# Performance work log

Measured on AMD Instinct MI355X. Metric: run time of the kernel, lower is better.

Reference implementation:

```python
import jax, jax.numpy as jnp
import numpy as np
import math

EMBED_DIM = 1024
NUM_HEADS = 16
HEAD_DIM = EMBED_DIM // NUM_HEADS
SCALING = HEAD_DIM ** -0.5
SOFTPLUS_BETA = math.log(2.0)


def linear(x, W, b):
    # torch nn.Linear: x @ W.T + b
    return jnp.einsum('...i,oi->...o', x, W) + b


def efficient_causal_attention_parallel(x, y, z):
    # x: (B, n, d1), y: (B, n, d1), z: (B, n, d2)
    n = x.shape[1]
    # outer products per step, then causal prefix-sum over n
    accum = jnp.cumsum(jnp.einsum('bni,bnj->bnij', y, z), axis=1)  # (B, n, d1, d2)
    res = jnp.einsum('bni,bnij->bnj', x, accum)                    # (B, n, d2)
    length_div = jnp.arange(1, n + 1, dtype=x.dtype)[None, :, None]
    return res / length_div


def setup_inputs() -> dict:
    key = jax.random.key(0)
    ks = jax.random.split(key, 12)
    tgt_len, bsz, plen = 2048, 2, 32
    E = EMBED_DIM
    s = 1.0 / math.sqrt(E)
    return {
        'query': jax.random.normal(ks[0], (tgt_len, bsz, E), jnp.float32),
        'pquery': jax.random.normal(ks[1], (plen, bsz, E), jnp.float32),
        'Wpq': jax.random.normal(ks[2], (E, E), jnp.float32) * s,
        'bpq': jnp.zeros((E,), jnp.float32),
        'Wq': jax.random.normal(ks[3], (E, E), jnp.float32) * s,
        'bq': jnp.zeros((E,), jnp.float32),
        'Wpc': jax.random.normal(ks[4], (E, E), jnp.float32) * s,
        'bpc': jnp.zeros((E,), jnp.float32),
        'Wc': jax.random.normal(ks[5], (E, E), jnp.float32) * s,
        'bc': jnp.zeros((E,), jnp.float32),
        'Wo': jax.random.normal(ks[6], (E, E), jnp.float32) * s,
        'bo': jnp.zeros((E,), jnp.float32),
    }


def reference(query, pquery, Wpq, bpq, Wq, bq, Wpc, bpc, Wc, bc, Wo, bo):
    tgt_len, bsz, E = query.shape
    plen = pquery.shape[0]
    H, D = NUM_HEADS, HEAD_DIM
    BH = bsz * H

    # pq: (plen, bsz, E) -> (bsz, H, plen, D), scaled
    pq = linear(pquery, Wpq, bpq).reshape(plen, bsz, H, D)
    pq = jnp.transpose(pq, (1, 2, 0, 3)) * SCALING

    # _compute_pattention: k (BH, tgt_len, D) @ pq^T (BH, D, plen)
    kp = linear(query, Wpc, bpc).reshape(tgt_len, BH, D).transpose(1, 0, 2)
    pqm = pq.reshape(BH, plen, D).transpose(0, 2, 1)  # (BH, D, plen)
    pattn = jnp.matmul(kp, pqm)                        # (BH, tgt_len, plen)
    pattn = jax.nn.softplus(SOFTPLUS_BETA * pattn) / SOFTPLUS_BETA

    q = (linear(query, Wq, bq) * SCALING).reshape(tgt_len, BH, D).transpose(1, 0, 2)
    kv = linear(query, Wc, bc).reshape(tgt_len, BH, D).transpose(1, 0, 2)  # tied k=v

    attn_weights = efficient_causal_attention_parallel(q, kv, pattn)  # (BH, tgt_len, plen)
    attn_weights = jax.nn.softmax(attn_weights, axis=-1)
    attn = efficient_causal_attention_parallel(attn_weights, pattn, kv)  # (BH, tgt_len, D)

    attn = attn.transpose(1, 0, 2).reshape(tgt_len, bsz, E)
    return linear(attn, Wo, bo)
```

## Files before the change

### kernel.cpp

```cpp
#include <hip/hip_runtime.h>
#include <hip/hip_bf16.h>
#include <math.h>

typedef __hip_bfloat16 bf16;
typedef __attribute__((ext_vector_type(8))) short bf16x8;
typedef __attribute__((ext_vector_type(4))) float f32x4;

__device__ __forceinline__ float bfbits(unsigned int u){ union{unsigned int x; float f;} c; c.x = u; return c.f; }
__device__ __forceinline__ short f2bf_s(float v){ union{ bf16 b; short s;} u; u.b = __float2bfloat16(v); return u.s; }

__device__ __forceinline__ void gl_lds16(const bf16* g, short* l) {
    __builtin_amdgcn_global_load_lds(
        (const __attribute__((address_space(1))) void*)g,
        (__attribute__((address_space(3))) void*)l, 16, 0, 0);
}

#define LN2F 0.69314718055994531f

__device__ __forceinline__ void cvt_store4(bf16* d, size_t idx, float4 v) {
    union { ushort4 u; bf16 b[4]; } o;
    o.b[0] = __float2bfloat16(v.x);
    o.b[1] = __float2bfloat16(v.y);
    o.b[2] = __float2bfloat16(v.z);
    o.b[3] = __float2bfloat16(v.w);
    ((ushort4*)d)[idx] = o.u;
}

__global__ __launch_bounds__(256)
void conv1_kernel(const float* __restrict__ query, const float* __restrict__ pquery,
                  const float* __restrict__ Wpq, bf16* __restrict__ qbf,
                  bf16* __restrict__ pqy, bf16* __restrict__ wpq)
{
    int blk = blockIdx.x;
    const float* s; bf16* d; int i;
    if (blk < 4096)      { s = query;  d = qbf; i = blk * 256 + threadIdx.x; }
    else if (blk < 4160) { s = pquery; d = pqy; i = (blk - 4096) * 256 + threadIdx.x; }
    else                 { s = Wpq;    d = wpq; i = (blk - 4160) * 256 + threadIdx.x; }
    cvt_store4(d, i, ((const float4*)s)[i]);
}

__global__ __launch_bounds__(256)
void conv2_kernel(const float* __restrict__ Wpc, const float* __restrict__ Wq,
                  const float* __restrict__ Wc, const float* __restrict__ Wo,
                  const float* __restrict__ bpc, const float* __restrict__ bq,
                  const float* __restrict__ bc,
                  bf16* __restrict__ wcat, bf16* __restrict__ wo_bf,
                  float* __restrict__ biascat)
{
    int blk = blockIdx.x;
    if (blk < 3072) {
        const float* s = (blk < 1024) ? Wpc : ((blk < 2048) ? Wq : Wc);
        int rel = (blk & 1023) * 256 + threadIdx.x;
        bf16* d = wcat + (size_t)(blk >> 10) * 1048576;
        cvt_store4(d, rel, ((const float4*)s)[rel]);
    } else if (blk < 4096) {
        int rel = (blk - 3072) * 256 + threadIdx.x;
        cvt_store4(wo_bf, rel, ((const float4*)Wo)[rel]);
    } else {
        int i = (blk - 4096) * 256 + threadIdx.x;
        float v = (i < 1024) ? bpc[i] : ((i < 2048) ? bq[i - 1024] : bc[i - 2048]);
        biascat[i] = v;
    }
}

__global__ __launch_bounds__(256)
void gemm_bf16_nt(const bf16* __restrict__ A, const bf16* __restrict__ B,
                  const float* __restrict__ bias, float* __restrict__ C,
                  int M, int N, int K, float scale_all, float scale_mid)
{
    __shared__ short As[128 * 32];
    __shared__ short Bs[128 * 32];

    const int tid  = threadIdx.x;
    const int lane = tid & 63;
    const int wave = tid >> 6;
    const int m0 = blockIdx.y * 128;
    const int n0 = blockIdx.x * 128;
    const int wm = (wave >> 1) * 64;
    const int wn = (wave & 1) * 64;

    f32x4 acc[4][4] = {};

    const int c0 = tid, c1 = tid + 256;
    const int r0 = c0 >> 2, s0 = c0 & 3;
    const int r1 = c1 >> 2, s1 = c1 & 3;

    const int kb = lane >> 4;
    const int rr = lane & 15;

    for (int k0 = 0; k0 < K; k0 += 32) {
        __syncthreads();
        gl_lds16(A + (size_t)(m0 + r0) * K + k0 + s0 * 8, As + c0 * 8);
        gl_lds16(A + (size_t)(m0 + r1) * K + k0 + s1 * 8, As + c1 * 8);
        gl_lds16(B + (size_t)(n0 + r0) * K + k0 + s0 * 8, Bs + c0 * 8);
        gl_lds16(B + (size_t)(n0 + r1) * K + k0 + s1 * 8, Bs + c1 * 8);
        __syncthreads();

        bf16x8 af[4], bfr[4];
        #pragma unroll
        for (int mi = 0; mi < 4; ++mi)
            af[mi] = *(const bf16x8*)(As + (wm + mi * 16 + rr) * 32 + kb * 8);
        #pragma unroll
        for (int ni = 0; ni < 4; ++ni)
            bfr[ni] = *(const bf16x8*)(Bs + (wn + ni * 16 + rr) * 32 + kb * 8);
        #pragma unroll
        for (int mi = 0; mi < 4; ++mi)
            #pragma unroll
            for (int ni = 0; ni < 4; ++ni)
                acc[mi][ni] = __builtin_amdgcn_mfma_f32_16x16x32_bf16(
                    af[mi], bfr[ni], acc[mi][ni], 0, 0, 0);
    }

    const int col_l = lane & 15;
    const int row_q = lane >> 4;
    #pragma unroll
    for (int ni = 0; ni < 4; ++ni) {
        int col = n0 + wn + ni * 16 + col_l;
        float bb = bias[col];
        float sc = ((col >> 10) == 1) ? scale_mid : scale_all;
        #pragma unroll
        for (int mi = 0; mi < 4; ++mi) {
            #pragma unroll
            for (int r = 0; r < 4; ++r) {
                int row = m0 + wm + mi * 16 + row_q * 4 + r;
                C[(size_t)row * N + col] = sc * (acc[mi][ni][r] + bb);
            }
        }
    }
}

__global__ __launch_bounds__(256)
void gemm_pq_partial(const bf16* __restrict__ A, const bf16* __restrict__ B,
                     float* __restrict__ part)
{
    __shared__ short As[64 * 32];
    __shared__ short Bs[128 * 32];

    const int tid  = threadIdx.x;
    const int lane = tid & 63;
    const int wave = tid >> 6;
    const int n0 = blockIdx.x * 128;
    const int kslice = blockIdx.y;
    const int kbase = kslice * 128;

    f32x4 acc[4][2] = {};

    const int ra = tid >> 2, sa = tid & 3;
    const int c0 = tid, c1 = tid + 256;
    const int rb0 = c0 >> 2, sb0 = c0 & 3;
    const int rb1 = c1 >> 2, sb1 = c1 & 3;

    const int kb = lane >> 4;
    const int rr = lane & 15;

    for (int k0 = kbase; k0 < kbase + 128; k0 += 32) {
        __syncthreads();
        gl_lds16(A + (size_t)ra * 1024 + k0 + sa * 8, As + tid * 8);
        gl_lds16(B + (size_t)(n0 + rb0) * 1024 + k0 + sb0 * 8, Bs + c0 * 8);
        gl_lds16(B + (size_t)(n0 + rb1) * 1024 + k0 + sb1 * 8, Bs + c1 * 8);
        __syncthreads();

        bf16x8 af[4], bfr[2];
        #pragma unroll
        for (int mi = 0; mi < 4; ++mi)
            af[mi] = *(const bf16x8*)(As + (mi * 16 + rr) * 32 + kb * 8);
        #pragma unroll
        for (int ni = 0; ni < 2; ++ni)
            bfr[ni] = *(const bf16x8*)(Bs + (wave * 32 + ni * 16 + rr) * 32 + kb * 8);
        #pragma unroll
        for (int mi = 0; mi < 4; ++mi)
            #pragma unroll
            for (int ni = 0; ni < 2; ++ni)
                acc[mi][ni] = __builtin_amdgcn_mfma_f32_16x16x32_bf16(
                    af[mi], bfr[ni], acc[mi][ni], 0, 0, 0);
    }

    const int col_l = lane & 15;
    const int row_q = lane >> 4;
    float* dst = part + (size_t)kslice * 65536;
    #pragma unroll
    for (int ni = 0; ni < 2; ++ni) {
        int col = n0 + wave * 32 + ni * 16 + col_l;
        #pragma unroll
        for (int mi = 0; mi < 4; ++mi) {
            #pragma unroll
            for (int r = 0; r < 4; ++r) {
                int row = mi * 16 + row_q * 4 + r;
                dst[(size_t)row * 1024 + col] = acc[mi][ni][r];
            }
        }
    }
}

__global__ __launch_bounds__(256)
void pq_reduce(const float* __restrict__ part, const float* __restrict__ bias,
               float* __restrict__ pq)
{
    int gid = blockIdx.x * 256 + threadIdx.x;
    int n = gid & 1023;
    float s = bias[n];
    #pragma unroll
    for (int k = 0; k < 8; ++k) s += part[(size_t)k * 65536 + gid];
    pq[gid] = 0.125f * s;
}

__global__ __launch_bounds__(256)
void pattn_sum_kernel(const float* __restrict__ kp, const float* __restrict__ kv,
                      const float* __restrict__ pq, float* __restrict__ pattn,
                      float* __restrict__ Sbuf, int T, int ld)
{
    const int NCH = 32;
    const int c = blockIdx.x, bh = blockIdx.y;
    const int b = bh >> 4, h = bh & 15;
    const int t0 = c * 64;
    const int tid = threadIdx.x;
    __shared__ float pqs[32][65];
    __shared__ float kps[64][65];
    __shared__ float ps[64][33];
    float* kvs = &kps[0][0];

    #pragma unroll
    for (int l = 0; l < 8; ++l) {
        int idx = tid + l * 256;
        int p = idx >> 6, d = idx & 63;
        pqs[p][d] = pq[(size_t)(p * 2 + b) * 1024 + h * 64 + d];
    }
    #pragma unroll
    for (int l = 0; l < 16; ++l) {
        int idx = tid + l * 256;
        int t = idx >> 6, d = idx & 63;
        kps[t][d] = kp[(size_t)((t0 + t) * 2 + b) * ld + h * 64 + d];
    }
    __syncthreads();

    const int p = tid & 31, tb = tid >> 5;
    float spv[8];
    #pragma unroll
    for (int l = 0; l < 8; ++l) {
        int t = tb + l * 8;
        float dot = 0.f;
        for (int d = 0; d < 64; ++d) dot += kps[t][d] * pqs[p][d];
        float z = LN2F * dot;
        spv[l] = (fmaxf(z, 0.f) + log1pf(expf(-fabsf(z)))) / LN2F;
    }
    __syncthreads();

    #pragma unroll
    for (int l = 0; l < 8; ++l) {
        int t = tb + l * 8;
        ps[t][p] = spv[l];
        pattn[((size_t)bh * T + t0 + t) * 32 + p] = spv[l];
    }
    #pragma unroll
    for (int l = 0; l < 16; ++l) {
        int idx = tid + l * 256;
        int t = idx >> 6, d = idx & 63;
        kvs[t * 64 + d] = kv[(size_t)((t0 + t) * 2 + b) * ld + h * 64 + d];
    }
    __syncthreads();

    const int j = tid & 31;
    const int ib = tid >> 5;
    float acc[8] = {};
    for (int r = 0; r < 64; ++r) {
        float pj = ps[r][j];
        #pragma unroll
        for (int k = 0; k < 8; ++k) acc[k] += kvs[r * 64 + ib + 8 * k] * pj;
    }
    float* Sdst = Sbuf + ((size_t)bh * NCH + c) * 2048;
    #pragma unroll
    for (int k = 0; k < 8; ++k) Sdst[tid + k * 256] = acc[k];
}

__global__ __launch_bounds__(256)
void prefix_state_kernel(float* __restrict__ Sbuf)
{
    const int NCH = 32;
    int gid = blockIdx.x * 256 + threadIdx.x;
    int bh = gid >> 11, e = gid & 2047;
    float* p = Sbuf + (size_t)bh * NCH * 2048 + e;
    float run = 0.f;
    #pragma unroll
    for (int c = 0; c < NCH; ++c) {
        float t = p[c * 2048];
        p[c * 2048] = run;
        run += t;
    }
}

__global__ __launch_bounds__(256)
void chunk_attn(const float* __restrict__ qg, const float* __restrict__ kvg,
                const float* __restrict__ pg, const float* __restrict__ Sg,
                bf16* __restrict__ attn, int T, int ld)
{
    __shared__ short sm[30720];
    short* sQ   = sm;
    short* sKV  = sm + 4608;
    short* sKVT = sm + 9216;
    short* sW   = sm + 13824;
    short* sAW  = sm + 18432;
    short* sS   = sm + 20992;
    short* sST  = sm + 23552;
    short* sP   = sm + 25856;
    short* sPT  = sm + 28416;

    const int bh = blockIdx.y, c = blockIdx.x;
    const int b = bh >> 4, h = bh & 15;
    const int t0 = c * 64;
    const int tid = threadIdx.x;
    const int lane = tid & 63;
    const int wave = tid >> 6;
    const int rr = lane & 15;
    const int kb = lane >> 4;
    const int m0w = wave * 16;
    const float* Sblk = Sg + ((size_t)bh * 32 + c) * 2048;

    #pragma unroll
    for (int l = 0; l < 4; ++l) {
        int idx = tid + l * 256;
        int t = idx >> 4, d4 = (idx & 15) * 4;
        size_t g = (size_t)((t0 + t) * 2 + b) * ld + h * 64 + d4;
        float4 qv = *(const float4*)(qg + g);
        union { ushort4 u; short s[4]; bf16 bb[4]; } cq;
        cq.bb[0] = __float2bfloat16(qv.x);
        cq.bb[1] = __float2bfloat16(qv.y);
        cq.bb[2] = __float2bfloat16(qv.z);
        cq.bb[3] = __float2bfloat16(qv.w);
        *(ushort4*)(sQ + t * 72 + d4) = cq.u;
        float4 kvv = *(const float4*)(kvg + g);
        union { ushort4 u; short s[4]; bf16 bb[4]; } ck;
        ck.bb[0] = __float2bfloat16(kvv.x);
        ck.bb[1] = __float2bfloat16(kvv.y);
        ck.bb[2] = __float2bfloat16(kvv.z);
        ck.bb[3] = __float2bfloat16(kvv.w);
        *(ushort4*)(sKV + t * 72 + d4) = ck.u;
        #pragma unroll
        for (int i = 0; i < 4; ++i) sKVT[(d4 + i) * 72 + t] = ck.s[i];
    }
    #pragma unroll
    for (int l = 0; l < 2; ++l) {
        int idx = tid + l * 256;
        int i = idx >> 3, j4 = (idx & 7) * 4;
        float4 sv = *(const float4*)(Sblk + i * 32 + j4);
        union { ushort4 u; short s[4]; bf16 bb[4]; } cs;
        cs.bb[0] = __float2bfloat16(sv.x);
        cs.bb[1] = __float2bfloat16(sv.y);
        cs.bb[2] = __float2bfloat16(sv.z);
        cs.bb[3] = __float2bfloat16(sv.w);
        *(ushort4*)(sS + i * 40 + j4) = cs.u;
        #pragma unroll
        for (int k = 0; k < 4; ++k) sST[(j4 + k) * 72 + i] = cs.s[k];
        float4 pv = *(const float4*)(pg + ((size_t)bh * T + t0 + i) * 32 + j4);
        union { ushort4 u; short s[4]; bf16 bb[4]; } cp;
        cp.bb[0] = __float2bfloat16(pv.x);
        cp.bb[1] = __float2bfloat16(pv.y);
        cp.bb[2] = __float2bfloat16(pv.z);
        cp.bb[3] = __float2bfloat16(pv.w);
        *(ushort4*)(sP + i * 40 + j4) = cp.u;
        #pragma unroll
        for (int k = 0; k < 4; ++k) sPT[(j4 + k) * 72 + i] = cp.s[k];
    }
    __syncthreads();

    {
        bf16x8 aq0 = *(const bf16x8*)(sQ + (m0w + rr) * 72 + kb * 8);
        bf16x8 aq1 = *(const bf16x8*)(sQ + (m0w + rr) * 72 + 32 + kb * 8);
        f32x4 acc[4] = {};
        #pragma unroll
        for (int nt = 0; nt < 4; ++nt) {
            bf16x8 b0 = *(const bf16x8*)(sKV + (nt * 16 + rr) * 72 + kb * 8);
            bf16x8 b1 = *(const bf16x8*)(sKV + (nt * 16 + rr) * 72 + 32 + kb * 8);
            acc[nt] = __builtin_amdgcn_mfma_f32_16x16x32_bf16(aq0, b0, acc[nt], 0, 0, 0);
            acc[nt] = __builtin_amdgcn_mfma_f32_16x16x32_bf16(aq1, b1, acc[nt], 0, 0, 0);
        }
        #pragma unroll
        for (int nt = 0; nt < 4; ++nt)
            #pragma unroll
            for (int r = 0; r < 4; ++r) {
                int t = m0w + kb * 4 + r;
                int s = nt * 16 + rr;
                sW[t * 72 + s] = f2bf_s((s <= t) ? acc[nt][r] : 0.f);
            }
    }
    __syncthreads();

    {
        bf16x8 aq0 = *(const bf16x8*)(sQ + (m0w + rr) * 72 + kb * 8);
        bf16x8 aq1 = *(const bf16x8*)(sQ + (m0w + rr) * 72 + 32 + kb * 8);
        bf16x8 aw0 = *(const bf16x8*)(sW + (m0w + rr) * 72 + kb * 8);
        bf16x8 aw1 = *(const bf16x8*)(sW + (m0w + rr) * 72 + 32 + kb * 8);
        f32x4 acc[2] = {};
        #pragma unroll
        for (int nt = 0; nt < 2; ++nt) {
            bf16x8 bs0 = *(const bf16x8*)(sST + (nt * 16 + rr) * 72 + kb * 8);
            bf16x8 bs1 = *(const bf16x8*)(sST + (nt * 16 + rr) * 72 + 32 + kb * 8);
            bf16x8 bp0 = *(const bf16x8*)(sPT + (nt * 16 + rr) * 72 + kb * 8);
            bf16x8 bp1 = *(const bf16x8*)(sPT + (nt * 16 + rr) * 72 + 32 + kb * 8);
            acc[nt] = __builtin_amdgcn_mfma_f32_16x16x32_bf16(aq0, bs0, acc[nt], 0, 0, 0);
            acc[nt] = __builtin_amdgcn_mfma_f32_16x16x32_bf16(aq1, bs1, acc[nt], 0, 0, 0);
            acc[nt] = __builtin_amdgcn_mfma_f32_16x16x32_bf16(aw0, bp0, acc[nt], 0, 0, 0);
            acc[nt] = __builtin_amdgcn_mfma_f32_16x16x32_bf16(aw1, bp1, acc[nt], 0, 0, 0);
        }
        #pragma unroll
        for (int r = 0; r < 4; ++r) {
            int t = m0w + kb * 4 + r;
            float inv_len = 1.0f / (float)(t0 + t + 1);
            float v0 = acc[0][r] * inv_len;
            float v1 = acc[1][r] * inv_len;
            float m = fmaxf(v0, v1);
            m = fmaxf(m, __shfl_xor(m, 1));
            m = fmaxf(m, __shfl_xor(m, 2));
            m = fmaxf(m, __shfl_xor(m, 4));
            m = fmaxf(m, __shfl_xor(m, 8));
            float e0 = __expf(v0 - m), e1 = __expf(v1 - m);
            float s = e0 + e1;
            s += __shfl_xor(s, 1);
            s += __shfl_xor(s, 2);
            s += __shfl_xor(s, 4);
            s += __shfl_xor(s, 8);
            float rs = 1.0f / s;
            sAW[t * 40 + rr]      = f2bf_s(e0 * rs);
            sAW[t * 40 + 16 + rr] = f2bf_s(e1 * rs);
        }
    }
    __syncthreads();

    {
        bf16x8 aa = *(const bf16x8*)(sAW + (m0w + rr) * 40 + kb * 8);
        f32x4 acc[4] = {};
        #pragma unroll
        for (int nt = 0; nt < 4; ++nt) {
            bf16x8 bp = *(const bf16x8*)(sP + (nt * 16 + rr) * 40 + kb * 8);
            acc[nt] = __builtin_amdgcn_mfma_f32_16x16x32_bf16(aa, bp, acc[nt], 0, 0, 0);
        }
        __syncthreads();
        #pragma unroll
        for (int nt = 0; nt < 4; ++nt)
            #pragma unroll
            for (int r = 0; r < 4; ++r) {
                int t = m0w + kb * 4 + r;
                int s = nt * 16 + rr;
                sW[t * 72 + s] = f2bf_s((s <= t) ? acc[nt][r] : 0.f);
            }
    }
    __syncthreads();

    {
        bf16x8 aa  = *(const bf16x8*)(sAW + (m0w + rr) * 40 + kb * 8);
        bf16x8 ap0 = *(const bf16x8*)(sW + (m0w + rr) * 72 + kb * 8);
        bf16x8 ap1 = *(const bf16x8*)(sW + (m0w + rr) * 72 + 32 + kb * 8);
        f32x4 acc[4] = {};
        #pragma unroll
        for (int nt = 0; nt < 4; ++nt) {
            bf16x8 bs = *(const bf16x8*)(sS + (nt * 16 + rr) * 40 + kb * 8);
            bf16x8 bk0 = *(const bf16x8*)(sKVT + (nt * 16 + rr) * 72 + kb * 8);
            bf16x8 bk1 = *(const bf16x8*)(sKVT + (nt * 16 + rr) * 72 + 32 + kb * 8);
            acc[nt] = __builtin_amdgcn_mfma_f32_16x16x32_bf16(aa,  bs,  acc[nt], 0, 0, 0);
            acc[nt] = __builtin_amdgcn_mfma_f32_16x16x32_bf16(ap0, bk0, acc[nt], 0, 0, 0);
            acc[nt] = __builtin_amdgcn_mfma_f32_16x16x32_bf16(ap1, bk1, acc[nt], 0, 0, 0);
        }
        #pragma unroll
        for (int nt = 0; nt < 4; ++nt)
            #pragma unroll
            for (int r = 0; r < 4; ++r) {
                int t = m0w + kb * 4 + r;
                int d = nt * 16 + rr;
                float v = acc[nt][r] / (float)(t0 + t + 1);
                ((unsigned short*)attn)[((size_t)((t0 + t) * 2 + b)) * 1024 + h * 64 + d] =
                    (unsigned short)f2bf_s(v);
            }
    }
}

extern "C" void kernel_launch(void* const* d_in, const int* in_sizes, int n_in,
                              void* d_out, int out_size, void* d_ws, size_t ws_size,
                              hipStream_t stream) {
    const float* query  = (const float*)d_in[0];
    const float* pquery = (const float*)d_in[1];
    const float* Wpq = (const float*)d_in[2];
    const float* bpq = (const float*)d_in[3];
    const float* Wq  = (const float*)d_in[4];
    const float* bq  = (const float*)d_in[5];
    const float* Wpc = (const float*)d_in[6];
    const float* bpc = (const float*)d_in[7];
    const float* Wc  = (const float*)d_in[8];
    const float* bc  = (const float*)d_in[9];
    const float* Wo  = (const float*)d_in[10];
    const float* bo  = (const float*)d_in[11];
    float* out = (float*)d_out;

    const int T = 2048, E = 1024, MROWS = 4096;
    const int NCH = 32;

    float* ws = (float*)d_ws;
    float* pq_buf    = ws;
    float* Cbig      = pq_buf + 65536;
    float* pattn_buf = Cbig + 12582912;
    float* S_buf     = pattn_buf + 2097152;
    float* qbf_f     = S_buf + 2097152;
    float* wcat_f    = qbf_f + 2097152;
    float* wo_f      = wcat_f + 1572864;

    bf16* qbf     = (bf16*)qbf_f;
    bf16* wcat    = (bf16*)wcat_f;
    bf16* wpq_bf  = (bf16*)wcat_f;
    bf16* wo_bf   = (bf16*)wo_f;
    bf16* pqy_bf  = (bf16*)pattn_buf;
    float* biascat = pattn_buf + 32768;
    float* pq_part = S_buf;
    bf16* attn_bf = qbf;

    conv1_kernel<<<5184, 256, 0, stream>>>(query, pquery, Wpq, qbf, pqy_bf, wpq_bf);
    gemm_pq_partial<<<dim3(8, 8), 256, 0, stream>>>(pqy_bf, wpq_bf, pq_part);
    pq_reduce<<<256, 256, 0, stream>>>(pq_part, bpq, pq_buf);

    conv2_kernel<<<4108, 256, 0, stream>>>(Wpc, Wq, Wc, Wo, bpc, bq, bc, wcat, wo_bf, biascat);

    gemm_bf16_nt<<<dim3(24, 32), 256, 0, stream>>>(
        qbf, wcat, biascat, Cbig, MROWS, 3072, E, 1.0f, 0.125f);

    pattn_sum_kernel<<<dim3(NCH, 32), 256, 0, stream>>>(
        Cbig, Cbig + 2048, pq_buf, pattn_buf, S_buf, T, 3072);
    prefix_state_kernel<<<256, 256, 0, stream>>>(S_buf);
    chunk_attn<<<dim3(NCH, 32), 256, 0, stream>>>(
        Cbig + 1024, Cbig + 2048, pattn_buf, S_buf, attn_bf, T, 3072);
    gemm_bf16_nt<<<dim3(8, 32), 256, 0, stream>>>(
        attn_bf, wo_bf, bo, out, MROWS, E, E, 1.0f, 1.0f);
}
```

Before: 228.7 us.

## Store projections and pattn in bf16, use MFMA in pattn_sum kernel

The fused QKV projection GEMM now writes bf16 instead of fp32, and pq and pattn are stored as bf16 too. This halves the intermediate traffic and removes the fp32-to-bf16 conversions at load time in chunk_attn. pattn_sum_kernel is rewritten so that both the kp·pq dot products and the per-chunk state sum run on bf16 MFMA with 16-byte vector loads, replacing the scalar fp32 loops. The cost is extra rounding of intermediates (kp, pattn, state inputs) to bf16, which lowers accuracy.

After: 198.8 us. 1.15x faster.

```diff
diff --git a/kernel.cpp b/kernel.cpp
--- a/kernel.cpp
+++ b/kernel.cpp
@@ -6,7 +6,6 @@
 typedef __attribute__((ext_vector_type(8))) short bf16x8;
 typedef __attribute__((ext_vector_type(4))) float f32x4;
 
-__device__ __forceinline__ float bfbits(unsigned int u){ union{unsigned int x; float f;} c; c.x = u; return c.f; }
 __device__ __forceinline__ short f2bf_s(float v){ union{ bf16 b; short s;} u; u.b = __float2bfloat16(v); return u.s; }
 
 __device__ __forceinline__ void gl_lds16(const bf16* g, short* l) {
@@ -25,6 +24,9 @@
     o.b[3] = __float2bfloat16(v.w);
     ((ushort4*)d)[idx] = o.u;
 }
+
+__device__ __forceinline__ void st_out(float* p, float v){ *p = v; }
+__device__ __forceinline__ void st_out(bf16* p, float v){ *p = __float2bfloat16(v); }
 
 __global__ __launch_bounds__(256)
 void conv1_kernel(const float* __restrict__ query, const float* __restrict__ pquery,
@@ -63,9 +65,10 @@
     }
 }
 
+template<typename TO>
 __global__ __launch_bounds__(256)
 void gemm_bf16_nt(const bf16* __restrict__ A, const bf16* __restrict__ B,
-                  const float* __restrict__ bias, float* __restrict__ C,
+                  const float* __restrict__ bias, TO* __restrict__ C,
                   int M, int N, int K, float scale_all, float scale_mid)
 {
     __shared__ short As[128 * 32];
@@ -123,7 +126,7 @@
             #pragma unroll
             for (int r = 0; r < 4; ++r) {
                 int row = m0 + wm + mi * 16 + row_q * 4 + r;
-                C[(size_t)row * N + col] = sc * (acc[mi][ni][r] + bb);
+                st_out(C + (size_t)row * N + col, sc * (acc[mi][ni][r] + bb));
             }
         }
     }
@@ -194,82 +197,100 @@
 
 __global__ __launch_bounds__(256)
 void pq_reduce(const float* __restrict__ part, const float* __restrict__ bias,
-               float* __restrict__ pq)
+               bf16* __restrict__ pq)
 {
     int gid = blockIdx.x * 256 + threadIdx.x;
     int n = gid & 1023;
     float s = bias[n];
     #pragma unroll
     for (int k = 0; k < 8; ++k) s += part[(size_t)k * 65536 + gid];
-    pq[gid] = 0.125f * s;
-}
-
-__global__ __launch_bounds__(256)
-void pattn_sum_kernel(const float* __restrict__ kp, const float* __restrict__ kv,
-                      const float* __restrict__ pq, float* __restrict__ pattn,
+    pq[gid] = __float2bfloat16(0.125f * s);
+}
+
+__global__ __launch_bounds__(256)
+void pattn_sum_kernel(const bf16* __restrict__ kp, const bf16* __restrict__ kv,
+                      const bf16* __restrict__ pqb, bf16* __restrict__ pattn,
                       float* __restrict__ Sbuf, int T, int ld)
 {
-    const int NCH = 32;
+    __shared__ short sKP[64 * 72];
+    __shared__ short sKVT[64 * 72];
+    __shared__ short sPQ[32 * 72];
+    __shared__ short sPT[32 * 72];
+
     const int c = blockIdx.x, bh = blockIdx.y;
     const int b = bh >> 4, h = bh & 15;
     const int t0 = c * 64;
     const int tid = threadIdx.x;
-    __shared__ float pqs[32][65];
-    __shared__ float kps[64][65];
-    __shared__ float ps[64][33];
-    float* kvs = &kps[0][0];
+    const int lane = tid & 63, wave = tid >> 6;
+    const int rr = lane & 15, kb = lane >> 4;
+    const int m0w = wave * 16;
 
     #pragma unroll
-    for (int l = 0; l < 8; ++l) {
+    for (int l = 0; l < 2; ++l) {
         int idx = tid + l * 256;
-        int p = idx >> 6, d = idx & 63;
-        pqs[p][d] = pq[(size_t)(p * 2 + b) * 1024 + h * 64 + d];
-    }
-    #pragma unroll
-    for (int l = 0; l < 16; ++l) {
-        int idx = tid + l * 256;
-        int t = idx >> 6, d = idx & 63;
-        kps[t][d] = kp[(size_t)((t0 + t) * 2 + b) * ld + h * 64 + d];
+        int t = idx >> 3, d8 = (idx & 7) * 8;
+        size_t g = (size_t)((t0 + t) * 2 + b) * ld + h * 64 + d8;
+        uint4 vk = *(const uint4*)(kp + g);
+        *(uint4*)(sKP + t * 72 + d8) = vk;
+        uint4 vv = *(const uint4*)(kv + g + 2048);
+        union { uint4 u; short s[8]; } cw; cw.u = vv;
+        #pragma unroll
+        for (int i = 0; i < 8; ++i) sKVT[(d8 + i) * 72 + t] = cw.s[i];
+    }
+    {
+        int p = tid >> 3, d8 = (tid & 7) * 8;
+        uint4 v = *(const uint4*)(pqb + (size_t)(p * 2 + b) * 1024 + h * 64 + d8);
+        *(uint4*)(sPQ + p * 72 + d8) = v;
     }
     __syncthreads();
 
-    const int p = tid & 31, tb = tid >> 5;
-    float spv[8];
-    #pragma unroll
-    for (int l = 0; l < 8; ++l) {
-        int t = tb + l * 8;
-        float dot = 0.f;
-        for (int d = 0; d < 64; ++d) dot += kps[t][d] * pqs[p][d];
-        float z = LN2F * dot;
-        spv[l] = (fmaxf(z, 0.f) + log1pf(expf(-fabsf(z)))) / LN2F;
+    {
+        bf16x8 a0 = *(const bf16x8*)(sKP + (m0w + rr) * 72 + kb * 8);
+        bf16x8 a1 = *(const bf16x8*)(sKP + (m0w + rr) * 72 + 32 + kb * 8);
+        f32x4 acc[2] = {};
+        #pragma unroll
+        for (int nt = 0; nt < 2; ++nt) {
+            bf16x8 b0 = *(const bf16x8*)(sPQ + (nt * 16 + rr) * 72 + kb * 8);
+            bf16x8 b1 = *(const bf16x8*)(sPQ + (nt * 16 + rr) * 72 + 32 + kb * 8);
+            acc[nt] = __builtin_amdgcn_mfma_f32_16x16x32_bf16(a0, b0, acc[nt], 0, 0, 0);
+            acc[nt] = __builtin_amdgcn_mfma_f32_16x16x32_bf16(a1, b1, acc[nt], 0, 0, 0);
+        }
+        #pragma unroll
+        for (int nt = 0; nt < 2; ++nt)
+            #pragma unroll
+            for (int r = 0; r < 4; ++r) {
+                int t = m0w + kb * 4 + r;
+                int p = nt * 16 + rr;
+                float z = LN2F * acc[nt][r];
+                float sp = (fmaxf(z, 0.f) + log1pf(__expf(-fabsf(z)))) / LN2F;
+                short sb = f2bf_s(sp);
+                sPT[p * 72 + t] = sb;
+                ((unsigned short*)pattn)[((size_t)bh * T + t0 + t) * 32 + p] = (unsigned short)sb;
+            }
     }
     __syncthreads();
 
-    #pragma unroll
-    for (int l = 0; l < 8; ++l) {
-        int t = tb + l * 8;
-        ps[t][p] = spv[l];
-        pattn[((size_t)bh * T + t0 + t) * 32 + p] = spv[l];
-    }
-    #pragma unroll
-    for (int l = 0; l < 16; ++l) {
-        int idx = tid + l * 256;
-        int t = idx >> 6, d = idx & 63;
-        kvs[t * 64 + d] = kv[(size_t)((t0 + t) * 2 + b) * ld + h * 64 + d];
-    }
-    __syncthreads();
-
-    const int j = tid & 31;
-    const int ib = tid >> 5;
-    float acc[8] = {};
-    for (int r = 0; r < 64; ++r) {
-        float pj = ps[r][j];
-        #pragma unroll
-        for (int k = 0; k < 8; ++k) acc[k] += kvs[r * 64 + ib + 8 * k] * pj;
-    }
-    float* Sdst = Sbuf + ((size_t)bh * NCH + c) * 2048;
-    #pragma unroll
-    for (int k = 0; k < 8; ++k) Sdst[tid + k * 256] = acc[k];
+    {
+        bf16x8 a0 = *(const bf16x8*)(sKVT + (m0w + rr) * 72 + kb * 8);
+        bf16x8 a1 = *(const bf16x8*)(sKVT + (m0w + rr) * 72 + 32 + kb * 8);
+        f32x4 acc[2] = {};
+        #pragma unroll
+        for (int nt = 0; nt < 2; ++nt) {
+            bf16x8 b0 = *(const bf16x8*)(sPT + (nt * 16 + rr) * 72 + kb * 8);
+            bf16x8 b1 = *(const bf16x8*)(sPT + (nt * 16 + rr) * 72 + 32 + kb * 8);
+            acc[nt] = __builtin_amdgcn_mfma_f32_16x16x32_bf16(a0, b0, acc[nt], 0, 0, 0);
+            acc[nt] = __builtin_amdgcn_mfma_f32_16x16x32_bf16(a1, b1, acc[nt], 0, 0, 0);
+        }
+        float* Sdst = Sbuf + ((size_t)bh * 32 + c) * 2048;
+        #pragma unroll
+        for (int nt = 0; nt < 2; ++nt)
+            #pragma unroll
+            for (int r = 0; r < 4; ++r) {
+                int i = m0w + kb * 4 + r;
+                int j = nt * 16 + rr;
+                Sdst[i * 32 + j] = acc[nt][r];
+            }
+    }
 }
 
 __global__ __launch_bounds__(256)
@@ -289,8 +310,8 @@
 }
 
 __global__ __launch_bounds__(256)
-void chunk_attn(const float* __restrict__ qg, const float* __restrict__ kvg,
-                const float* __restrict__ pg, const float* __restrict__ Sg,
+void chunk_attn(const bf16* __restrict__ qg, const bf16* __restrict__ kvg,
+                const bf16* __restrict__ pg, const float* __restrict__ Sg,
                 bf16* __restrict__ attn, int T, int ld)
 {
     __shared__ short sm[30720];
@@ -316,49 +337,43 @@
     const float* Sblk = Sg + ((size_t)bh * 32 + c) * 2048;
 
     #pragma unroll
-    for (int l = 0; l < 4; ++l) {
-        int idx = tid + l * 256;
-        int t = idx >> 4, d4 = (idx & 15) * 4;
-        size_t g = (size_t)((t0 + t) * 2 + b) * ld + h * 64 + d4;
-        float4 qv = *(const float4*)(qg + g);
-        union { ushort4 u; short s[4]; bf16 bb[4]; } cq;
-        cq.bb[0] = __float2bfloat16(qv.x);
-        cq.bb[1] = __float2bfloat16(qv.y);
-        cq.bb[2] = __float2bfloat16(qv.z);
-        cq.bb[3] = __float2bfloat16(qv.w);
-        *(ushort4*)(sQ + t * 72 + d4) = cq.u;
-        float4 kvv = *(const float4*)(kvg + g);
-        union { ushort4 u; short s[4]; bf16 bb[4]; } ck;
-        ck.bb[0] = __float2bfloat16(kvv.x);
-        ck.bb[1] = __float2bfloat16(kvv.y);
-        ck.bb[2] = __float2bfloat16(kvv.z);
-        ck.bb[3] = __float2bfloat16(kvv.w);
-        *(ushort4*)(sKV + t * 72 + d4) = ck.u;
-        #pragma unroll
-        for (int i = 0; i < 4; ++i) sKVT[(d4 + i) * 72 + t] = ck.s[i];
-    }
-    #pragma unroll
     for (int l = 0; l < 2; ++l) {
         int idx = tid + l * 256;
-        int i = idx >> 3, j4 = (idx & 7) * 4;
-        float4 sv = *(const float4*)(Sblk + i * 32 + j4);
-        union { ushort4 u; short s[4]; bf16 bb[4]; } cs;
-        cs.bb[0] = __float2bfloat16(sv.x);
-        cs.bb[1] = __float2bfloat16(sv.y);
-        cs.bb[2] = __float2bfloat16(sv.z);
-        cs.bb[3] = __float2bfloat16(sv.w);
-        *(ushort4*)(sS + i * 40 + j4) = cs.u;
-        #pragma unroll
-        for (int k = 0; k < 4; ++k) sST[(j4 + k) * 72 + i] = cs.s[k];
-        float4 pv = *(const float4*)(pg + ((size_t)bh * T + t0 + i) * 32 + j4);
-        union { ushort4 u; short s[4]; bf16 bb[4]; } cp;
-        cp.bb[0] = __float2bfloat16(pv.x);
-        cp.bb[1] = __float2bfloat16(pv.y);
-        cp.bb[2] = __float2bfloat16(pv.z);
-        cp.bb[3] = __float2bfloat16(pv.w);
-        *(ushort4*)(sP + i * 40 + j4) = cp.u;
-        #pragma unroll
-        for (int k = 0; k < 4; ++k) sPT[(j4 + k) * 72 + i] = cp.s[k];
+        int t = idx >> 3, d8 = (idx & 7) * 8;
+        size_t g = (size_t)((t0 + t) * 2 + b) * ld + h * 64 + d8;
+        uint4 qv = *(const uint4*)(qg + g);
+        *(uint4*)(sQ + t * 72 + d8) = qv;
+        uint4 kvv = *(const uint4*)(kvg + g);
+        *(uint4*)(sKV + t * 72 + d8) = kvv;
+        union { uint4 u; short s[8]; } ck; ck.u = kvv;
+        #pragma unroll
+        for (int i = 0; i < 8; ++i) sKVT[(d8 + i) * 72 + t] = ck.s[i];
+    }
+    {
+        int t = tid >> 2, j8 = (tid & 3) * 8;
+        uint4 pv = *(const uint4*)(pg + ((size_t)bh * T + t0 + t) * 32 + j8);
+        *(uint4*)(sP + t * 40 + j8) = pv;
+        union { uint4 u; short s[8]; } cp; cp.u = pv;
+        #pragma unroll
+        for (int i = 0; i < 8; ++i) sPT[(j8 + i) * 72 + t] = cp.s[i];
+
+        float4 s0 = *(const float4*)(Sblk + t * 32 + j8);
+        float4 s1 = *(const float4*)(Sblk + t * 32 + j8 + 4);
+        union { ushort4 u; short s[4]; bf16 bb[4]; } c0, c1;
+        c0.bb[0] = __float2bfloat16(s0.x);
+        c0.bb[1] = __float2bfloat16(s0.y);
+        c0.bb[2] = __float2bfloat16(s0.z);
+        c0.bb[3] = __float2bfloat16(s0.w);
+        c1.bb[0] = __float2bfloat16(s1.x);
+        c1.bb[1] = __float2bfloat16(s1.y);
+        c1.bb[2] = __float2bfloat16(s1.z);
+        c1.bb[3] = __float2bfloat16(s1.w);
+        *(ushort4*)(sS + t * 40 + j8) = c0.u;
+        *(ushort4*)(sS + t * 40 + j8 + 4) = c1.u;
+        #pragma unroll
+        for (int i = 0; i < 4; ++i) sST[(j8 + i) * 72 + t] = c0.s[i];
+        #pragma unroll
+        for (int i = 0; i < 4; ++i) sST[(j8 + 4 + i) * 72 + t] = c1.s[i];
     }
     __syncthreads();
 
@@ -493,37 +508,40 @@
     const int NCH = 32;
 
     float* ws = (float*)d_ws;
-    float* pq_buf    = ws;
-    float* Cbig      = pq_buf + 65536;
-    float* pattn_buf = Cbig + 12582912;
-    float* S_buf     = pattn_buf + 2097152;
+    float* pq_f      = ws;
+    float* Cbig_f    = pq_f + 65536;
+    float* pattn_f   = Cbig_f + 6291456;
+    float* S_buf     = pattn_f + 1048576;
     float* qbf_f     = S_buf + 2097152;
     float* wcat_f    = qbf_f + 2097152;
     float* wo_f      = wcat_f + 1572864;
 
+    bf16* pq_bf   = (bf16*)pq_f;
+    bf16* Cbig    = (bf16*)Cbig_f;
+    bf16* pattn_bf= (bf16*)pattn_f;
     bf16* qbf     = (bf16*)qbf_f;
     bf16* wcat    = (bf16*)wcat_f;
     bf16* wpq_bf  = (bf16*)wcat_f;
     bf16* wo_bf   = (bf16*)wo_f;
-    bf16* pqy_bf  = (bf16*)pattn_buf;
-    float* biascat = pattn_buf + 32768;
+    bf16* pqy_bf  = (bf16*)pattn_f;
+    float* biascat = pattn_f + 32768;
     float* pq_part = S_buf;
     bf16* attn_bf = qbf;
 
     conv1_kernel<<<5184, 256, 0, stream>>>(query, pquery, Wpq, qbf, pqy_bf, wpq_bf);
     gemm_pq_partial<<<dim3(8, 8), 256, 0, stream>>>(pqy_bf, wpq_bf, pq_part);
-    pq_reduce<<<256, 256, 0, stream>>>(pq_part, bpq, pq_buf);
+    pq_reduce<<<256, 256, 0, stream>>>(pq_part, bpq, pq_bf);
 
     conv2_kernel<<<4108, 256, 0, stream>>>(Wpc, Wq, Wc, Wo, bpc, bq, bc, wcat, wo_bf, biascat);
 
-    gemm_bf16_nt<<<dim3(24, 32), 256, 0, stream>>>(
+    gemm_bf16_nt<bf16><<<dim3(24, 32), 256, 0, stream>>>(
         qbf, wcat, biascat, Cbig, MROWS, 3072, E, 1.0f, 0.125f);
 
     pattn_sum_kernel<<<dim3(NCH, 32), 256, 0, stream>>>(
-        Cbig, Cbig + 2048, pq_buf, pattn_buf, S_buf, T, 3072);
+        Cbig, Cbig, pq_bf, pattn_bf, S_buf, T, 3072);
     prefix_state_kernel<<<256, 256, 0, stream>>>(S_buf);
     chunk_attn<<<dim3(NCH, 32), 256, 0, stream>>>(
-        Cbig + 1024, Cbig + 2048, pattn_buf, S_buf, attn_bf, T, 3072);
-    gemm_bf16_nt<<<dim3(8, 32), 256, 0, stream>>>(
+        Cbig + 1024, Cbig + 2048, pattn_bf, S_buf, attn_bf, T, 3072);
+    gemm_bf16_nt<float><<<dim3(8, 32), 256, 0, stream>>>(
         attn_bf, wo_bf, bo, out, MROWS, E, E, 1.0f, 1.0f);
 }
```
